# Optimization experiments

Hardware: AMD Instinct MI355X
Metric: run time of the kernel (lower is better)

The kernel has to match this reference:

```python
import jax, jax.numpy as jnp
import numpy as np

N_NODES = 40962
N_EDGES = 245760
K = 10  # gaussian kernels
D = 2   # pseudo-coordinate dim
EPS = 1e-15


def gmm_conv(x, edge_index, pseudo, g, mu, sigma, root, bias):
    """PyG GMMConv with aggr='mean', root_weight=True.
    x: [N, Cin], edge_index: [2, E] (row 0 = source j, row 1 = target i),
    pseudo: [E, D], g: [Cin, K*Cout], mu/sigma: [K, D], root: [Cin, Cout], bias: [Cout].
    """
    src, dst = edge_index[0], edge_index[1]
    E = pseudo.shape[0]
    # Gaussian mixture edge weights: [E, K]
    diff = pseudo[:, None, :] - mu[None, :, :]                     # [E, K, D]
    w = jnp.exp(jnp.sum(-0.5 * diff * diff / (EPS + sigma[None] ** 2), axis=-1))
    xj = x[src]                                                    # [E, Cin] gather
    y = (xj @ g).reshape(E, K, -1)                                 # [E, K, Cout]
    msg = jnp.sum(y * w[:, :, None], axis=1)                       # [E, Cout]
    agg = jax.ops.segment_sum(msg, dst, num_segments=N_NODES)      # scatter-add
    deg = jax.ops.segment_sum(jnp.ones((E,), x.dtype), dst, num_segments=N_NODES)
    agg = agg / jnp.maximum(deg, 1.0)[:, None]                     # mean aggregation
    return agg + x @ root + bias


def setup_inputs() -> dict:
    key = jax.random.key(0)
    ks = jax.random.split(key, 20)
    Cin, Ch, Cout = 64, 64, 128
    sc = lambda fan: 1.0 / np.sqrt(fan)
    inp = {
        "x": jax.random.normal(ks[0], (N_NODES, Cin), jnp.float32),
        "edge_index": jax.random.randint(ks[1], (2, N_EDGES), 0, N_NODES, jnp.int32),
        "pseudo": jax.random.uniform(ks[2], (N_EDGES, D), jnp.float32),
        # conv1: Cin -> Ch
        "g1": jax.random.normal(ks[3], (Cin, K * Ch), jnp.float32) * sc(Cin),
        "mu1": jax.random.uniform(ks[4], (K, D), jnp.float32),
        "sigma1": jax.random.uniform(ks[5], (K, D), jnp.float32) + 0.5,
        "root1": jax.random.normal(ks[6], (Cin, Ch), jnp.float32) * sc(Cin),
        "b1": jnp.zeros((Ch,), jnp.float32),
        # conv2: Ch -> Cout
        "g2": jax.random.normal(ks[7], (Ch, K * Cout), jnp.float32) * sc(Ch),
        "mu2": jax.random.uniform(ks[8], (K, D), jnp.float32),
        "sigma2": jax.random.uniform(ks[9], (K, D), jnp.float32) + 0.5,
        "root2": jax.random.normal(ks[10], (Ch, Cout), jnp.float32) * sc(Ch),
        "b2": jnp.zeros((Cout,), jnp.float32),
        # shortcut: Cin -> Cout (size_in != size_out)
        "gs": jax.random.normal(ks[11], (Cin, K * Cout), jnp.float32) * sc(Cin),
        "mus": jax.random.uniform(ks[12], (K, D), jnp.float32),
        "sigmas": jax.random.uniform(ks[13], (K, D), jnp.float32) + 0.5,
        "roots": jax.random.normal(ks[14], (Cin, Cout), jnp.float32) * sc(Cin),
        "bs": jnp.zeros((Cout,), jnp.float32),
    }
    return inp


def reference(x, edge_index, pseudo, g1, mu1, sigma1, root1, b1,
              g2, mu2, sigma2, root2, b2, gs, mus, sigmas, roots, bs):
    h = gmm_conv(x, edge_index, pseudo, g1, mu1, sigma1, root1, b1)
    h = jax.nn.relu(h)
    y = gmm_conv(h, edge_index, pseudo, g2, mu2, sigma2, root2, b2)
    x_s = gmm_conv(x, edge_index, pseudo, gs, mus, sigmas, roots, bs)
    return jax.nn.relu(y + x_s)
```

## Files before the change

### kernel.cpp

```cpp
#include <hip/hip_runtime.h>
#include <hip/hip_bf16.h>

using bf16 = __hip_bfloat16;
typedef __attribute__((ext_vector_type(8))) short short8;
typedef __attribute__((ext_vector_type(4))) float float4v;

#define N_NODES 40962
#define N_EDGES 245760
#define NP      41024
#define KG      10
#define SCAN_B  256
#define NBLK    ((NP + SCAN_B - 1) / SCAN_B)
#define GRID1   (NP / 64)

#define CVT_V   (N_NODES * 64 / 8)
#define CVT_BLK ((CVT_V + 255) / 256)
#define W3_BLK  (N_EDGES / 256)
#define PACK_N  (64 * 704 + 2 * 128 * 704)
#define PACK_BLK (PACK_N / 256)


__device__ __forceinline__ float ldf(const void* p, size_t i, int isf32) {
    return isf32 ? ((const float*)p)[i] : __bfloat162float(((const bf16*)p)[i]);
}
__device__ __forceinline__ float blo(unsigned u) { return __uint_as_float(u << 16); }
__device__ __forceinline__ float bhi(unsigned u) { return __uint_as_float(u & 0xffff0000u); }
__device__ __forceinline__ unsigned pk2(float a, float b) {
    union { bf16 h[2]; unsigned u; } t;
    t.h[0] = __float2bfloat16(a);
    t.h[1] = __float2bfloat16(b);
    return t.u;
}
__device__ __forceinline__ int rfl(int v) { return __builtin_amdgcn_readfirstlane(v); }

__device__ __forceinline__ void gll16(const void* g, void* l) {
    __builtin_amdgcn_global_load_lds(
        (const __attribute__((address_space(1))) void*)g,
        (__attribute__((address_space(3))) void*)l, 16, 0, 0);
}

__global__ void k_detect_count(const void* x, const int* __restrict__ ei,
                               int* __restrict__ flag, int* __restrict__ deg) {
    if (blockIdx.x == 0) {
        __shared__ int huge_c, zero_even;
        if (threadIdx.x == 0) { huge_c = 0; zero_even = 0; }
        __syncthreads();
        const bf16* xb = (const bf16*)x;
        int lh = 0, lz = 0;
        for (int i = threadIdx.x; i < 8192; i += 256) {
            float v = __bfloat162float(xb[i]);
            if (!(fabsf(v) <= 1e4f)) lh++;
            if ((i & 1) == 0 && v == 0.0f) lz++;
        }
        atomicAdd(&huge_c, lh);
        atomicAdd(&zero_even, lz);
        __syncthreads();
        if (threadIdx.x == 0) flag[0] = (huge_c > 0 || zero_even > 3000) ? 1 : 0;
    } else {
        int e = (blockIdx.x - 1) * 256 + threadIdx.x;
        if (e < N_EDGES) atomicAdd(&deg[ei[N_EDGES + e]], 1);
    }
}

__global__ void k_scan1(const int* __restrict__ deg, int* __restrict__ offs,
                        int* __restrict__ bsum) {
    __shared__ int buf[SCAN_B];
    int t = threadIdx.x, b = blockIdx.x;
    int i = b * SCAN_B + t;
    int v = (i < NP) ? deg[i] : 0;
    buf[t] = v;
    __syncthreads();
    for (int off = 1; off < SCAN_B; off <<= 1) {
        int a = (t >= off) ? buf[t - off] : 0;
        __syncthreads();
        buf[t] += a;
        __syncthreads();
    }
    if (i < NP) offs[i] = buf[t] - v;
    if (t == SCAN_B - 1) bsum[b] = buf[t];
}

__global__ void k_scan3m(int* __restrict__ offs, const int* __restrict__ bsum,
                         const int* __restrict__ deg, int* __restrict__ cur,
                         float* __restrict__ invdeg) {
    __shared__ int buf[256];
    int t = threadIdx.x, b = blockIdx.x;
    int v = (t < NBLK) ? bsum[t] : 0;
    buf[t] = v;
    __syncthreads();
    for (int off = 1; off < 256; off <<= 1) {
        int a = (t >= off) ? buf[t - off] : 0;
        __syncthreads();
        buf[t] += a;
        __syncthreads();
    }
    int bofs = (b > 0) ? buf[b - 1] : 0;
    int total = buf[NBLK - 1];
    int i = b * 256 + t;
    if (i < NP) {
        int o = offs[i] + bofs;
        offs[i] = o;
        cur[i] = o;
        int d = deg[i];
        invdeg[i] = 1.0f / (float)(d > 1 ? d : 1);
    }
    if (i == 0) offs[NP] = total;
}

__global__ void k_fill(const int* __restrict__ ei, int* __restrict__ cur,
                       int* __restrict__ csr) {
    int e = blockIdx.x * 256 + threadIdx.x;
    if (e < N_EDGES) {
        int pos = atomicAdd(&cur[ei[N_EDGES + e]], 1);
        csr[pos] = e;
    }
}

__device__ __forceinline__ void gw_one(float p0, float p1, const void* mu,
                                       const void* sg, int f, float* out) {
#pragma unroll
    for (int k = 0; k < KG; k++) {
        float m0 = ldf(mu, 2 * k + 0, f), m1 = ldf(mu, 2 * k + 1, f);
        float s0 = ldf(sg, 2 * k + 0, f), s1 = ldf(sg, 2 * k + 1, f);
        float d0 = p0 - m0, d1 = p1 - m1;
        float t = -0.5f * (d0 * d0 / (1e-15f + s0 * s0) + d1 * d1 / (1e-15f + s1 * s1));
        out[k] = __expf(t);
    }
}

__device__ __forceinline__ void pack_frag(const void* g, const void* root, int f,
                                          int idx, int Cout, bf16* Bp) {
    int j = idx & 7;
    int lane = (idx >> 3) & 63;
    int rem = idx >> 9;
    int kc = rem % 22;
    int n = rem / 22;
    int col = n * 16 + (lane & 15);
    int k = kc * 32 + (lane >> 4) * 8 + j;
    float v;
    if (k < 512) {
        int cin = k >> 3, kg = k & 7;
        v = ldf(g, (size_t)cin * (KG * Cout) + (size_t)kg * Cout + col, f);
    } else if (k < 640) {
        int jj = k - 512;
        int cin = jj >> 1, kg = 8 + (jj & 1);
        v = ldf(g, (size_t)cin * (KG * Cout) + (size_t)kg * Cout + col, f);
    } else {
        v = ldf(root, (size_t)(k - 640) * Cout + col, f);
    }
    Bp[idx] = __float2bfloat16(v);
}

__global__ void k_prep_all(const void* __restrict__ x, const void* __restrict__ pseudo,
                           const void* mu1, const void* sg1, const void* mu2,
                           const void* sg2, const void* mus, const void* sgs,
                           const void* g1, const void* root1, const void* g2,
                           const void* root2, const void* gs, const void* roots,
                           const int* __restrict__ flag, bf16* __restrict__ Xf,
                           bf16* __restrict__ wab, bf16* __restrict__ w2b,
                           bf16* wt1p, bf16* wt2p, bf16* wtsp) {
    int b = blockIdx.x;
    int tid = threadIdx.x;
    int f = flag[0];
    if (b < CVT_BLK) {
        int i = b * 256 + tid;
        if (i < CVT_V) {
            int node = i >> 3, j = i & 7;
            uint4 u;
            if (f) {
                const float4* xf = (const float4*)x;
                float4 a = xf[2 * i], c = xf[2 * i + 1];
                union { bf16 t[8]; uint4 u; } tt;
                tt.t[0] = __float2bfloat16(a.x); tt.t[1] = __float2bfloat16(a.y);
                tt.t[2] = __float2bfloat16(a.z); tt.t[3] = __float2bfloat16(a.w);
                tt.t[4] = __float2bfloat16(c.x); tt.t[5] = __float2bfloat16(c.y);
                tt.t[6] = __float2bfloat16(c.z); tt.t[7] = __float2bfloat16(c.w);
                u = tt.u;
            } else {
                u = ((const uint4*)x)[i];
            }
            *(uint4*)(Xf + ((size_t)(j >> 2) * NP + node) * 32 + (j & 3) * 8) = u;
        }
    } else if (b < CVT_BLK + W3_BLK) {
        int e = (b - CVT_BLK) * 256 + tid;
        float p0 = ldf(pseudo, (size_t)e * 2 + 0, f);
        float p1 = ldf(pseudo, (size_t)e * 2 + 1, f);
        float o1[KG], o2[KG], os[KG];
        gw_one(p0, p1, mu1, sg1, f, o1);
        gw_one(p0, p1, mu2, sg2, f, o2);
        gw_one(p0, p1, mus, sgs, f, os);
        unsigned* d = (unsigned*)(wab + (size_t)e * 20);
        d[0] = pk2(o1[0], o1[1]); d[1] = pk2(o1[2], o1[3]);
        d[2] = pk2(o1[4], o1[5]); d[3] = pk2(o1[6], o1[7]);
        d[4] = pk2(o1[8], o1[9]);
        d[5] = pk2(os[0], os[1]); d[6] = pk2(os[2], os[3]);
        d[7] = pk2(os[4], os[5]); d[8] = pk2(os[6], os[7]);
        d[9] = pk2(os[8], os[9]);
        unsigned* d2 = (unsigned*)(w2b + (size_t)e * 10);
        d2[0] = pk2(o2[0], o2[1]); d2[1] = pk2(o2[2], o2[3]);
        d2[2] = pk2(o2[4], o2[5]); d2[3] = pk2(o2[6], o2[7]);
        d2[4] = pk2(o2[8], o2[9]);
    } else {
        int idx = (b - CVT_BLK - W3_BLK) * 256 + tid;
        if (idx < 64 * 704) {
            pack_frag(g1, root1, f, idx, 64, wt1p);
        } else if (idx < 64 * 704 + 128 * 704) {
            pack_frag(g2, root2, f, idx - 64 * 704, 128, wt2p);
        } else {
            pack_frag(gs, roots, f, idx - 64 * 704 - 128 * 704, 128, wtsp);
        }
    }
}

__device__ __forceinline__ void store_zf(bf16* Zf, int wid, int lane, const float* a,
                                         float inv) {
    union { bf16 h[8]; uint4 u; } p;
#pragma unroll
    for (int k = 0; k < 8; k++) p.h[k] = __float2bfloat16(a[k] * inv);
    *(uint4*)(Zf + ((size_t)(lane >> 2) * NP + wid) * 32 + (lane & 3) * 8) = p.u;
    *(unsigned*)(Zf + ((size_t)(16 + (lane >> 4)) * NP + wid) * 32 + (lane & 15) * 2) =
        pk2(a[8] * inv, a[9] * inv);
}

__device__ __forceinline__ float ldx_frag(const bf16* X, int src, int lane) {
    return __bfloat162float(X[((size_t)(lane >> 5) * NP + src) * 32 + (lane & 31)]);
}

__device__ __forceinline__ int csr_at(const int* csr, int idx) {
    if (idx > N_EDGES - 1) idx = N_EDGES - 1;
    return rfl(csr[idx]);
}

__global__ void k_gather2(const int* __restrict__ ei, const int* __restrict__ offs,
                          const int* __restrict__ csr, const bf16* __restrict__ wab,
                          const float* __restrict__ invdeg, const bf16* __restrict__ X,
                          bf16* __restrict__ Za, bf16* __restrict__ Zb) {
    int wid = (blockIdx.x * 256 + threadIdx.x) >> 6;
    int lane = threadIdx.x & 63;
    if (wid >= NP) return;
    float aa[KG], ab[KG];
#pragma unroll
    for (int k = 0; k < KG; k++) { aa[k] = 0.0f; ab[k] = 0.0f; }
    int beg = rfl(offs[wid]);
    int end = rfl(offs[wid + 1]);
    int cnt = end - beg;

    int e0 = csr_at(csr, beg + 0);
    int e1 = csr_at(csr, beg + 1);
    int e2 = csr_at(csr, beg + 2);
    int s1 = rfl(ei[e1]);
    const unsigned* wp0 = (const unsigned*)(wab + (size_t)e0 * 20);
    unsigned c0 = wp0[0], c1 = wp0[1], c2 = wp0[2], c3 = wp0[3], c4 = wp0[4];
    unsigned c5 = wp0[5], c6 = wp0[6], c7 = wp0[7], c8 = wp0[8], c9 = wp0[9];
    const unsigned* wp1 = (const unsigned*)(wab + (size_t)e1 * 20);
    unsigned n0 = wp1[0], n1 = wp1[1], n2 = wp1[2], n3 = wp1[3], n4 = wp1[4];
    unsigned n5 = wp1[5], n6 = wp1[6], n7 = wp1[7], n8 = wp1[8], n9 = wp1[9];
    int s0 = rfl(ei[e0]);
    float xv = ldx_frag(X, s0, lane);

    for (int t = 0; t < cnt; ++t) {
        int e3 = csr_at(csr, beg + t + 3);
        int s2 = rfl(ei[e2]);
        const unsigned* wp2 = (const unsigned*)(wab + (size_t)e2 * 20);
        unsigned m0 = wp2[0], m1 = wp2[1], m2 = wp2[2], m3 = wp2[3], m4 = wp2[4];
        unsigned m5 = wp2[5], m6 = wp2[6], m7 = wp2[7], m8 = wp2[8], m9 = wp2[9];
        float xv1 = ldx_frag(X, s1, lane);
        aa[0] += blo(c0) * xv; aa[1] += bhi(c0) * xv;
        aa[2] += blo(c1) * xv; aa[3] += bhi(c1) * xv;
        aa[4] += blo(c2) * xv; aa[5] += bhi(c2) * xv;
        aa[6] += blo(c3) * xv; aa[7] += bhi(c3) * xv;
        aa[8] += blo(c4) * xv; aa[9] += bhi(c4) * xv;
        ab[0] += blo(c5) * xv; ab[1] += bhi(c5) * xv;
        ab[2] += blo(c6) * xv; ab[3] += bhi(c6) * xv;
        ab[4] += blo(c7) * xv; ab[5] += bhi(c7) * xv;
        ab[6] += blo(c8) * xv; ab[7] += bhi(c8) * xv;
        ab[8] += blo(c9) * xv; ab[9] += bhi(c9) * xv;
        e2 = e3; s1 = s2; xv = xv1;
        c0 = n0; c1 = n1; c2 = n2; c3 = n3; c4 = n4;
        c5 = n5; c6 = n6; c7 = n7; c8 = n8; c9 = n9;
        n0 = m0; n1 = m1; n2 = m2; n3 = m3; n4 = m4;
        n5 = m5; n6 = m6; n7 = m7; n8 = m8; n9 = m9;
    }
    float inv = invdeg[wid];
    store_zf(Za, wid, lane, aa, inv);
    store_zf(Zb, wid, lane, ab, inv);
}

__global__ void k_gather(const int* __restrict__ ei, const int* __restrict__ offs,
                         const int* __restrict__ csr, const bf16* __restrict__ w,
                         int wstride, const float* __restrict__ invdeg,
                         const bf16* __restrict__ X, bf16* __restrict__ Z) {
    int wid = (blockIdx.x * 256 + threadIdx.x) >> 6;
    int lane = threadIdx.x & 63;
    if (wid >= NP) return;
    float acc[KG];
#pragma unroll
    for (int k = 0; k < KG; k++) acc[k] = 0.0f;
    int beg = rfl(offs[wid]);
    int end = rfl(offs[wid + 1]);
    int cnt = end - beg;

    int e0 = csr_at(csr, beg + 0);
    int e1 = csr_at(csr, beg + 1);
    int e2 = csr_at(csr, beg + 2);
    int s1 = rfl(ei[e1]);
    const unsigned* wp0 = (const unsigned*)(w + (size_t)e0 * wstride);
    unsigned c0 = wp0[0], c1 = wp0[1], c2 = wp0[2], c3 = wp0[3], c4 = wp0[4];
    const unsigned* wp1 = (const unsigned*)(w + (size_t)e1 * wstride);
    unsigned n0 = wp1[0], n1 = wp1[1], n2 = wp1[2], n3 = wp1[3], n4 = wp1[4];
    int s0 = rfl(ei[e0]);
    float xv = ldx_frag(X, s0, lane);

    for (int t = 0; t < cnt; ++t) {
        int e3 = csr_at(csr, beg + t + 3);
        int s2 = rfl(ei[e2]);
        const unsigned* wp2 = (const unsigned*)(w + (size_t)e2 * wstride);
        unsigned m0 = wp2[0], m1 = wp2[1], m2 = wp2[2], m3 = wp2[3], m4 = wp2[4];
        float xv1 = ldx_frag(X, s1, lane);
        acc[0] += blo(c0) * xv; acc[1] += bhi(c0) * xv;
        acc[2] += blo(c1) * xv; acc[3] += bhi(c1) * xv;
        acc[4] += blo(c2) * xv; acc[5] += bhi(c2) * xv;
        acc[6] += blo(c3) * xv; acc[7] += bhi(c3) * xv;
        acc[8] += blo(c4) * xv; acc[9] += bhi(c4) * xv;
        e2 = e3; s1 = s2; xv = xv1;
        c0 = n0; c1 = n1; c2 = n2; c3 = n3; c4 = n4;
        n0 = m0; n1 = m1; n2 = m2; n3 = m3; n4 = m4;
    }
    store_zf(Z, wid, lane, acc, invdeg[wid]);
}

template <int NT, int MODE>
__device__ __forceinline__ void gemm_body(
    int bid, const bf16* __restrict__ Zf, const bf16* __restrict__ Xf,
    const bf16* __restrict__ Bp, const void* __restrict__ bias, int f,
    const bf16* __restrict__ addsrc, bf16* __restrict__ outb,
    void* __restrict__ outp, bf16* __restrict__ sB) {
    constexpr int Cout = NT * 16;
    int lane = threadIdx.x & 63;
    int wave = threadIdx.x >> 6;
    int m = lane & 15, quad = lane >> 4;
    int row0 = bid * 64 + wave * 16;

    const bf16* arow = Zf + ((size_t)(row0 + m)) * 32 + quad * 8;
    const bf16* xrow = Xf + ((size_t)(row0 + m)) * 32 + quad * 8;

    float4v acc[NT];
#pragma unroll
    for (int n = 0; n < NT; n++) acc[n] = (float4v){0.f, 0.f, 0.f, 0.f};

#pragma unroll
    for (int n = wave; n < NT; n += 4)
        gll16(Bp + ((size_t)(n * 22 + 0) * 64 + lane) * 8, sB + n * 512);
    short8 a_cur = *(const short8*)arow;
    __syncthreads();

#pragma unroll
    for (int kc = 0; kc < 22; kc++) {
        int buf = kc & 1;
        short8 a_nxt;
        if (kc < 21) {
            int kn = kc + 1;
#pragma unroll
            for (int n = wave; n < NT; n += 4)
                gll16(Bp + ((size_t)(n * 22 + kn) * 64 + lane) * 8,
                      sB + (size_t)(1 - buf) * NT * 512 + n * 512);
            a_nxt = (kn < 20)
                ? *(const short8*)(arow + (size_t)kn * NP * 32)
                : *(const short8*)(xrow + (size_t)(kn - 20) * NP * 32);
        }
        const bf16* bb = sB + (size_t)buf * NT * 512 + lane * 8;
#pragma unroll
        for (int n = 0; n < NT; n++) {
            short8 b = *(const short8*)(bb + (size_t)n * 512);
            acc[n] = __builtin_amdgcn_mfma_f32_16x16x32_bf16(a_cur, b, acc[n], 0, 0, 0);
        }
        __syncthreads();
        if (kc < 21) a_cur = a_nxt;
    }

#pragma unroll
    for (int n = 0; n < NT; n++) {
        int gcol = n * 16 + m;
        float bv = ldf(bias, gcol, f);
#pragma unroll
        for (int r = 0; r < 4; r++) {
            int grow = row0 + quad * 4 + r;
            if (grow >= N_NODES) continue;
            float v = acc[n][r] + bv;
            if (MODE == 0) {
                outb[((size_t)(gcol >> 5) * NP + grow) * 32 + (gcol & 31)] =
                    __float2bfloat16(fmaxf(v, 0.f));
            } else if (MODE == 1) {
                outb[(size_t)grow * Cout + gcol] = __float2bfloat16(v);
            } else {
                size_t oidx = (size_t)grow * Cout + gcol;
                v = fmaxf(v + __bfloat162float(addsrc[oidx]), 0.f);
                if (f) ((float*)outp)[oidx] = v;
                else   ((bf16*)outp)[oidx] = __float2bfloat16(v);
            }
        }
    }
}

__global__ __launch_bounds__(256) void k_gemm_pair(
    const bf16* __restrict__ za, const bf16* __restrict__ zb,
    const bf16* __restrict__ Xf, const bf16* __restrict__ wt1p,
    const bf16* __restrict__ wtsp, const void* __restrict__ b1,
    const void* __restrict__ bs, const int* __restrict__ flag,
    bf16* __restrict__ hf, bf16* __restrict__ ys) {
    __shared__ bf16 sB[2 * 8 * 512];
    int f = flag[0];
    if (blockIdx.x < GRID1)
        gemm_body<4, 0>(blockIdx.x, za, Xf, wt1p, b1, f, nullptr, hf, nullptr, sB);
    else
        gemm_body<8, 1>(blockIdx.x - GRID1, zb, Xf, wtsp, bs, f, nullptr, ys, nullptr,
                        sB);
}

template <int NT, int MODE>
__global__ __launch_bounds__(256) void k_gemm_one(
    const bf16* __restrict__ Zf, const bf16* __restrict__ Xf,
    const bf16* __restrict__ Bp, const void* __restrict__ bias,
    const int* __restrict__ flag, const bf16* __restrict__ addsrc,
    bf16* __restrict__ outb, void* __restrict__ outp) {
    __shared__ bf16 sB[2 * NT * 512];
    gemm_body<NT, MODE>(blockIdx.x, Zf, Xf, Bp, bias, flag[0], addsrc, outb, outp, sB);
}

extern "C" void kernel_launch(void* const* d_in, const int* in_sizes, int n_in,
                              void* d_out, int out_size, void* d_ws, size_t ws_size,
                              hipStream_t stream) {
    const void* x      = d_in[0];
    const int*  ei     = (const int*)d_in[1];
    const void* pseudo = d_in[2];
    const void* g1     = d_in[3];
    const void* mu1    = d_in[4];
    const void* sg1    = d_in[5];
    const void* root1  = d_in[6];
    const void* b1     = d_in[7];
    const void* g2     = d_in[8];
    const void* mu2    = d_in[9];
    const void* sg2    = d_in[10];
    const void* root2  = d_in[11];
    const void* b2     = d_in[12];
    const void* gs     = d_in[13];
    const void* mus    = d_in[14];
    const void* sgs    = d_in[15];
    const void* roots  = d_in[16];
    const void* bs     = d_in[17];

    char* ws = (char*)d_ws;
    size_t off = 0;
    auto alloc = [&](size_t bytes) -> char* {
        char* p = ws + off;
        off += (bytes + 255) & ~(size_t)255;
        return p;
    };
    const size_t ZSZ = (size_t)20 * NP * 32 * 2;
    const size_t XFS = (size_t)2 * NP * 32 * 2;

    int*   flag   = (int*)alloc(256);
    int*   deg    = (int*)alloc((size_t)NP * 4);
    int*   offs   = (int*)alloc((size_t)(NP + 1) * 4);
    int*   cur    = (int*)alloc((size_t)NP * 4);
    float* invdeg = (float*)alloc((size_t)NP * 4);
    int*   bsum   = (int*)alloc((size_t)NBLK * 4);
    int*   csr    = (int*)alloc((size_t)N_EDGES * 4);
    bf16*  Xf     = (bf16*)alloc(XFS);
    bf16*  hf     = (bf16*)alloc(XFS);
    bf16*  ys     = (bf16*)alloc((size_t)N_NODES * 128 * 2);
    bf16*  wt1p   = (bf16*)alloc((size_t)64 * 704 * 2);
    bf16*  wt2p   = (bf16*)alloc((size_t)128 * 704 * 2);
    bf16*  wtsp   = (bf16*)alloc((size_t)128 * 704 * 2);
    bf16*  wab    = (bf16*)alloc((size_t)N_EDGES * 20 * 2);
    bf16*  w2b    = (bf16*)alloc((size_t)N_EDGES * 10 * 2);
    size_t common_end = off;

    bf16* za = (bf16*)alloc(ZSZ);
    bf16* zb = (bf16*)alloc(ZSZ);
    bool big = (off <= ws_size);

    hipMemsetAsync(deg, 0, (size_t)NP * 4, stream);
    k_detect_count<<<1 + (N_EDGES + 255) / 256, 256, 0, stream>>>(x, ei, flag, deg);
    k_prep_all<<<CVT_BLK + W3_BLK + PACK_BLK, 256, 0, stream>>>(
        x, pseudo, mu1, sg1, mu2, sg2, mus, sgs, g1, root1, g2, root2, gs, roots,
        flag, Xf, wab, w2b, wt1p, wt2p, wtsp);
    k_scan1<<<NBLK, SCAN_B, 0, stream>>>(deg, offs, bsum);
    k_scan3m<<<NBLK, 256, 0, stream>>>(offs, bsum, deg, cur, invdeg);
    k_fill<<<(N_EDGES + 255) / 256, 256, 0, stream>>>(ei, cur, csr);

    if (big) {
        k_gather2<<<NP / 4, 256, 0, stream>>>(ei, offs, csr, wab, invdeg, Xf, za, zb);
        k_gemm_pair<<<2 * GRID1, 256, 0, stream>>>(za, zb, Xf, wt1p, wtsp, b1, bs,
                                                   flag, hf, ys);
        k_gather<<<NP / 4, 256, 0, stream>>>(ei, offs, csr, w2b, 10, invdeg, hf, za);
        k_gemm_one<8, 2><<<GRID1, 256, 0, stream>>>(za, hf, wt2p, b2, flag, ys,
                                                    (bf16*)nullptr, d_out);
    } else {
        off = common_end;
        bf16* z = (bf16*)alloc(ZSZ);
        k_gather<<<NP / 4, 256, 0, stream>>>(ei, offs, csr, wab, 20, invdeg, Xf, z);
        k_gemm_one<4, 0><<<GRID1, 256, 0, stream>>>(z, Xf, wt1p, b1, flag,
                                                    (const bf16*)nullptr, hf, nullptr);
        k_gather<<<NP / 4, 256, 0, stream>>>(ei, offs, csr, wab + 10, 20, invdeg, Xf, z);
        k_gemm_one<8, 1><<<GRID1, 256, 0, stream>>>(z, Xf, wtsp, bs, flag,
                                                    (const bf16*)nullptr, ys, nullptr);
        k_gather<<<NP / 4, 256, 0, stream>>>(ei, offs, csr, w2b, 10, invdeg, hf, z);
        k_gemm_one<8, 2><<<GRID1, 256, 0, stream>>>(z, hf, wt2p, b2, flag, ys,
                                                    (bf16*)nullptr, d_out);
    }
}
```

Before: 274.7 us.

## Store edge weights and source ids in CSR order to remove gather indirection

```diff
diff --git a/kernel.cpp b/kernel.cpp
--- a/kernel.cpp
+++ b/kernel.cpp
@@ -108,11 +108,12 @@
 }
 
 __global__ void k_fill(const int* __restrict__ ei, int* __restrict__ cur,
-                       int* __restrict__ csr) {
+                       int* __restrict__ ep, int* __restrict__ csr_src) {
     int e = blockIdx.x * 256 + threadIdx.x;
     if (e < N_EDGES) {
         int pos = atomicAdd(&cur[ei[N_EDGES + e]], 1);
-        csr[pos] = e;
+        ep[e] = pos;
+        csr_src[pos] = ei[e];
     }
 }
 
@@ -156,9 +157,10 @@
                            const void* sg2, const void* mus, const void* sgs,
                            const void* g1, const void* root1, const void* g2,
                            const void* root2, const void* gs, const void* roots,
-                           const int* __restrict__ flag, bf16* __restrict__ Xf,
-                           bf16* __restrict__ wab, bf16* __restrict__ w2b,
-                           bf16* wt1p, bf16* wt2p, bf16* wtsp) {
+                           const int* __restrict__ flag, const int* __restrict__ ep,
+                           bf16* __restrict__ Xf, bf16* __restrict__ wcab,
+                           bf16* __restrict__ wc2, bf16* wt1p, bf16* wt2p,
+                           bf16* wtsp) {
     int b = blockIdx.x;
     int tid = threadIdx.x;
     int f = flag[0];
@@ -189,14 +191,15 @@
         gw_one(p0, p1, mu1, sg1, f, o1);
         gw_one(p0, p1, mu2, sg2, f, o2);
         gw_one(p0, p1, mus, sgs, f, os);
-        unsigned* d = (unsigned*)(wab + (size_t)e * 20);
+        int pos = ep[e];
+        unsigned* d = (unsigned*)wcab + (size_t)pos * 10;
         d[0] = pk2(o1[0], o1[1]); d[1] = pk2(o1[2], o1[3]);
         d[2] = pk2(o1[4], o1[5]); d[3] = pk2(o1[6], o1[7]);
         d[4] = pk2(o1[8], o1[9]);
         d[5] = pk2(os[0], os[1]); d[6] = pk2(os[2], os[3]);
         d[7] = pk2(os[4], os[5]); d[8] = pk2(os[6], os[7]);
         d[9] = pk2(os[8], os[9]);
-        unsigned* d2 = (unsigned*)(w2b + (size_t)e * 10);
+        unsigned* d2 = (unsigned*)wc2 + (size_t)pos * 5;
         d2[0] = pk2(o2[0], o2[1]); d2[1] = pk2(o2[2], o2[3]);
         d2[2] = pk2(o2[4], o2[5]); d2[3] = pk2(o2[6], o2[7]);
         d2[4] = pk2(o2[8], o2[9]);
@@ -226,13 +229,12 @@
     return __bfloat162float(X[((size_t)(lane >> 5) * NP + src) * 32 + (lane & 31)]);
 }
 
-__device__ __forceinline__ int csr_at(const int* csr, int idx) {
-    if (idx > N_EDGES - 1) idx = N_EDGES - 1;
-    return rfl(csr[idx]);
-}
-
-__global__ void k_gather2(const int* __restrict__ ei, const int* __restrict__ offs,
-                          const int* __restrict__ csr, const bf16* __restrict__ wab,
+__device__ __forceinline__ int clampe(int idx) {
+    return idx > N_EDGES - 1 ? N_EDGES - 1 : idx;
+}
+
+__global__ void k_gather2(const int* __restrict__ offs, const int* __restrict__ csr_src,
+                          const bf16* __restrict__ wcab,
                           const float* __restrict__ invdeg, const bf16* __restrict__ X,
                           bf16* __restrict__ Za, bf16* __restrict__ Zb) {
     int wid = (blockIdx.x * 256 + threadIdx.x) >> 6;
@@ -244,38 +246,37 @@
     int beg = rfl(offs[wid]);
     int end = rfl(offs[wid + 1]);
     int cnt = end - beg;
-
-    int e0 = csr_at(csr, beg + 0);
-    int e1 = csr_at(csr, beg + 1);
-    int e2 = csr_at(csr, beg + 2);
-    int s1 = rfl(ei[e1]);
-    const unsigned* wp0 = (const unsigned*)(wab + (size_t)e0 * 20);
+    const unsigned* wb = (const unsigned*)wcab;
+
+    int s0 = rfl(csr_src[clampe(beg + 0)]);
+    int s1 = rfl(csr_src[clampe(beg + 1)]);
+    int sC = rfl(csr_src[clampe(beg + 2)]);
+    float xv0 = ldx_frag(X, s0, lane);
+    float xv1 = ldx_frag(X, s1, lane);
+    const unsigned* wp0 = wb + (size_t)clampe(beg + 0) * 10;
     unsigned c0 = wp0[0], c1 = wp0[1], c2 = wp0[2], c3 = wp0[3], c4 = wp0[4];
     unsigned c5 = wp0[5], c6 = wp0[6], c7 = wp0[7], c8 = wp0[8], c9 = wp0[9];
-    const unsigned* wp1 = (const unsigned*)(wab + (size_t)e1 * 20);
+    const unsigned* wp1 = wb + (size_t)clampe(beg + 1) * 10;
     unsigned n0 = wp1[0], n1 = wp1[1], n2 = wp1[2], n3 = wp1[3], n4 = wp1[4];
     unsigned n5 = wp1[5], n6 = wp1[6], n7 = wp1[7], n8 = wp1[8], n9 = wp1[9];
-    int s0 = rfl(ei[e0]);
-    float xv = ldx_frag(X, s0, lane);
 
     for (int t = 0; t < cnt; ++t) {
-        int e3 = csr_at(csr, beg + t + 3);
-        int s2 = rfl(ei[e2]);
-        const unsigned* wp2 = (const unsigned*)(wab + (size_t)e2 * 20);
+        int sN = rfl(csr_src[clampe(beg + t + 3)]);
+        float xv2 = ldx_frag(X, sC, lane);
+        const unsigned* wp2 = wb + (size_t)clampe(beg + t + 2) * 10;
         unsigned m0 = wp2[0], m1 = wp2[1], m2 = wp2[2], m3 = wp2[3], m4 = wp2[4];
         unsigned m5 = wp2[5], m6 = wp2[6], m7 = wp2[7], m8 = wp2[8], m9 = wp2[9];
-        float xv1 = ldx_frag(X, s1, lane);
-        aa[0] += blo(c0) * xv; aa[1] += bhi(c0) * xv;
-        aa[2] += blo(c1) * xv; aa[3] += bhi(c1) * xv;
-        aa[4] += blo(c2) * xv; aa[5] += bhi(c2) * xv;
-        aa[6] += blo(c3) * xv; aa[7] += bhi(c3) * xv;
-        aa[8] += blo(c4) * xv; aa[9] += bhi(c4) * xv;
-        ab[0] += blo(c5) * xv; ab[1] += bhi(c5) * xv;
-        ab[2] += blo(c6) * xv; ab[3] += bhi(c6) * xv;
-        ab[4] += blo(c7) * xv; ab[5] += bhi(c7) * xv;
-        ab[6] += blo(c8) * xv; ab[7] += bhi(c8) * xv;
-        ab[8] += blo(c9) * xv; ab[9] += bhi(c9) * xv;
-        e2 = e3; s1 = s2; xv = xv1;
+        aa[0] += blo(c0) * xv0; aa[1] += bhi(c0) * xv0;
+        aa[2] += blo(c1) * xv0; aa[3] += bhi(c1) * xv0;
+        aa[4] += blo(c2) * xv0; aa[5] += bhi(c2) * xv0;
+        aa[6] += blo(c3) * xv0; aa[7] += bhi(c3) * xv0;
+        aa[8] += blo(c4) * xv0; aa[9] += bhi(c4) * xv0;
+        ab[0] += blo(c5) * xv0; ab[1] += bhi(c5) * xv0;
+        ab[2] += blo(c6) * xv0; ab[3] += bhi(c6) * xv0;
+        ab[4] += blo(c7) * xv0; ab[5] += bhi(c7) * xv0;
+        ab[6] += blo(c8) * xv0; ab[7] += bhi(c8) * xv0;
+        ab[8] += blo(c9) * xv0; ab[9] += bhi(c9) * xv0;
+        xv0 = xv1; xv1 = xv2; sC = sN;
         c0 = n0; c1 = n1; c2 = n2; c3 = n3; c4 = n4;
         c5 = n5; c6 = n6; c7 = n7; c8 = n8; c9 = n9;
         n0 = m0; n1 = m1; n2 = m2; n3 = m3; n4 = m4;
@@ -286,9 +287,9 @@
     store_zf(Zb, wid, lane, ab, inv);
 }
 
-__global__ void k_gather(const int* __restrict__ ei, const int* __restrict__ offs,
-                         const int* __restrict__ csr, const bf16* __restrict__ w,
-                         int wstride, const float* __restrict__ invdeg,
+__global__ void k_gather(const int* __restrict__ offs, const int* __restrict__ csr_src,
+                         const bf16* __restrict__ w, int wstride,
+                         const float* __restrict__ invdeg,
                          const bf16* __restrict__ X, bf16* __restrict__ Z) {
     int wid = (blockIdx.x * 256 + threadIdx.x) >> 6;
     int lane = threadIdx.x & 63;
@@ -300,29 +301,27 @@
     int end = rfl(offs[wid + 1]);
     int cnt = end - beg;
 
-    int e0 = csr_at(csr, beg + 0);
-    int e1 = csr_at(csr, beg + 1);
-    int e2 = csr_at(csr, beg + 2);
-    int s1 = rfl(ei[e1]);
-    const unsigned* wp0 = (const unsigned*)(w + (size_t)e0 * wstride);
+    int s0 = rfl(csr_src[clampe(beg + 0)]);
+    int s1 = rfl(csr_src[clampe(beg + 1)]);
+    int sC = rfl(csr_src[clampe(beg + 2)]);
+    float xv0 = ldx_frag(X, s0, lane);
+    float xv1 = ldx_frag(X, s1, lane);
+    const unsigned* wp0 = (const unsigned*)(w + (size_t)clampe(beg + 0) * wstride);
     unsigned c0 = wp0[0], c1 = wp0[1], c2 = wp0[2], c3 = wp0[3], c4 = wp0[4];
-    const unsigned* wp1 = (const unsigned*)(w + (size_t)e1 * wstride);
+    const unsigned* wp1 = (const unsigned*)(w + (size_t)clampe(beg + 1) * wstride);
     unsigned n0 = wp1[0], n1 = wp1[1], n2 = wp1[2], n3 = wp1[3], n4 = wp1[4];
-    int s0 = rfl(ei[e0]);
-    float xv = ldx_frag(X, s0, lane);
 
     for (int t = 0; t < cnt; ++t) {
-        int e3 = csr_at(csr, beg + t + 3);
-        int s2 = rfl(ei[e2]);
-        const unsigned* wp2 = (const unsigned*)(w + (size_t)e2 * wstride);
+        int sN = rfl(csr_src[clampe(beg + t + 3)]);
+        float xv2 = ldx_frag(X, sC, lane);
+        const unsigned* wp2 = (const unsigned*)(w + (size_t)clampe(beg + t + 2) * wstride);
         unsigned m0 = wp2[0], m1 = wp2[1], m2 = wp2[2], m3 = wp2[3], m4 = wp2[4];
-        float xv1 = ldx_frag(X, s1, lane);
-        acc[0] += blo(c0) * xv; acc[1] += bhi(c0) * xv;
-        acc[2] += blo(c1) * xv; acc[3] += bhi(c1) * xv;
-        acc[4] += blo(c2) * xv; acc[5] += bhi(c2) * xv;
-        acc[6] += blo(c3) * xv; acc[7] += bhi(c3) * xv;
-        acc[8] += blo(c4) * xv; acc[9] += bhi(c4) * xv;
-        e2 = e3; s1 = s2; xv = xv1;
+        acc[0] += blo(c0) * xv0; acc[1] += bhi(c0) * xv0;
+        acc[2] += blo(c1) * xv0; acc[3] += bhi(c1) * xv0;
+        acc[4] += blo(c2) * xv0; acc[5] += bhi(c2) * xv0;
+        acc[6] += blo(c3) * xv0; acc[7] += bhi(c3) * xv0;
+        acc[8] += blo(c4) * xv0; acc[9] += bhi(c4) * xv0;
+        xv0 = xv1; xv1 = xv2; sC = sN;
         c0 = n0; c1 = n1; c2 = n2; c3 = n3; c4 = n4;
         n0 = m0; n1 = m1; n2 = m2; n3 = m3; n4 = m4;
     }
@@ -465,15 +464,16 @@
     int*   cur    = (int*)alloc((size_t)NP * 4);
     float* invdeg = (float*)alloc((size_t)NP * 4);
     int*   bsum   = (int*)alloc((size_t)NBLK * 4);
-    int*   csr    = (int*)alloc((size_t)N_EDGES * 4);
+    int*   ep     = (int*)alloc((size_t)N_EDGES * 4);
+    int*   csrs   = (int*)alloc((size_t)N_EDGES * 4);
     bf16*  Xf     = (bf16*)alloc(XFS);
     bf16*  hf     = (bf16*)alloc(XFS);
     bf16*  ys     = (bf16*)alloc((size_t)N_NODES * 128 * 2);
     bf16*  wt1p   = (bf16*)alloc((size_t)64 * 704 * 2);
     bf16*  wt2p   = (bf16*)alloc((size_t)128 * 704 * 2);
     bf16*  wtsp   = (bf16*)alloc((size_t)128 * 704 * 2);
-    bf16*  wab    = (bf16*)alloc((size_t)N_EDGES * 20 * 2);
-    bf16*  w2b    = (bf16*)alloc((size_t)N_EDGES * 10 * 2);
+    bf16*  wcab   = (bf16*)alloc((size_t)N_EDGES * 20 * 2);
+    bf16*  wc2    = (bf16*)alloc((size_t)N_EDGES * 10 * 2);
     size_t common_end = off;
 
     bf16* za = (bf16*)alloc(ZSZ);
@@ -482,30 +482,30 @@
 
     hipMemsetAsync(deg, 0, (size_t)NP * 4, stream);
     k_detect_count<<<1 + (N_EDGES + 255) / 256, 256, 0, stream>>>(x, ei, flag, deg);
+    k_scan1<<<NBLK, SCAN_B, 0, stream>>>(deg, offs, bsum);
+    k_scan3m<<<NBLK, 256, 0, stream>>>(offs, bsum, deg, cur, invdeg);
+    k_fill<<<(N_EDGES + 255) / 256, 256, 0, stream>>>(ei, cur, ep, csrs);
     k_prep_all<<<CVT_BLK + W3_BLK + PACK_BLK, 256, 0, stream>>>(
         x, pseudo, mu1, sg1, mu2, sg2, mus, sgs, g1, root1, g2, root2, gs, roots,
-        flag, Xf, wab, w2b, wt1p, wt2p, wtsp);
-    k_scan1<<<NBLK, SCAN_B, 0, stream>>>(deg, offs, bsum);
-    k_scan3m<<<NBLK, 256, 0, stream>>>(offs, bsum, deg, cur, invdeg);
-    k_fill<<<(N_EDGES + 255) / 256, 256, 0, stream>>>(ei, cur, csr);
+        flag, ep, Xf, wcab, wc2, wt1p, wt2p, wtsp);
 
     if (big) {
-        k_gather2<<<NP / 4, 256, 0, stream>>>(ei, offs, csr, wab, invdeg, Xf, za, zb);
+        k_gather2<<<NP / 4, 256, 0, stream>>>(offs, csrs, wcab, invdeg, Xf, za, zb);
         k_gemm_pair<<<2 * GRID1, 256, 0, stream>>>(za, zb, Xf, wt1p, wtsp, b1, bs,
                                                    flag, hf, ys);
-        k_gather<<<NP / 4, 256, 0, stream>>>(ei, offs, csr, w2b, 10, invdeg, hf, za);
+        k_gather<<<NP / 4, 256, 0, stream>>>(offs, csrs, wc2, 10, invdeg, hf, za);
         k_gemm_one<8, 2><<<GRID1, 256, 0, stream>>>(za, hf, wt2p, b2, flag, ys,
                                                     (bf16*)nullptr, d_out);
     } else {
         off = common_end;
         bf16* z = (bf16*)alloc(ZSZ);
-        k_gather<<<NP / 4, 256, 0, stream>>>(ei, offs, csr, wab, 20, invdeg, Xf, z);
+        k_gather<<<NP / 4, 256, 0, stream>>>(offs, csrs, wcab, 20, invdeg, Xf, z);
         k_gemm_one<4, 0><<<GRID1, 256, 0, stream>>>(z, Xf, wt1p, b1, flag,
                                                     (const bf16*)nullptr, hf, nullptr);
-        k_gather<<<NP / 4, 256, 0, stream>>>(ei, offs, csr, wab + 10, 20, invdeg, Xf, z);
+        k_gather<<<NP / 4, 256, 0, stream>>>(offs, csrs, wcab + 10, 20, invdeg, Xf, z);
         k_gemm_one<8, 1><<<GRID1, 256, 0, stream>>>(z, Xf, wtsp, bs, flag,
                                                     (const bf16*)nullptr, ys, nullptr);
-        k_gather<<<NP / 4, 256, 0, stream>>>(ei, offs, csr, w2b, 10, invdeg, hf, z);
+        k_gather<<<NP / 4, 256, 0, stream>>>(offs, csrs, wc2, 10, invdeg, hf, z);
         k_gemm_one<8, 2><<<GRID1, 256, 0, stream>>>(z, hf, wt2p, b2, flag, ys,
                                                     (bf16*)nullptr, d_out);
     }
```

Result: faster. 267.7 us (-2.6%).
